# Optimization experiments

Hardware: AMD Instinct MI355X
Metric: run time of the kernel (lower is better)

## Reference

```python
import jax, jax.numpy as jnp
from jax import lax
import numpy as np

B, D, L = 32, 64, 4096
E = 8          # num_experts
K = 2          # top-k
OC = 32        # out_channels


def setup_inputs() -> dict:
    key = jax.random.key(0)
    ks = jax.random.split(key, 6)
    x = jax.random.normal(ks[0], (B, D, L), dtype=jnp.float32)
    # gating weight [D*5, E] (torch init is zeros; use small random for a meaningful reference)
    w_gate = jax.random.normal(ks[1], (D * 5, E), dtype=jnp.float32) * 0.02
    # Conv1d(D -> OC, kernel 3)
    conv1_w = jax.random.normal(ks[2], (OC, D, 3), dtype=jnp.float32) * (1.0 / np.sqrt(D * 3))
    conv1_b = jax.random.normal(ks[3], (OC,), dtype=jnp.float32) * 0.01
    # Conv1d(OC -> OC*E, kernel 1)
    conv2_w = jax.random.normal(ks[4], (OC * E, OC, 1), dtype=jnp.float32) * (1.0 / np.sqrt(OC))
    conv2_b = jax.random.normal(ks[5], (OC * E,), dtype=jnp.float32) * 0.01
    return {"x": x, "w_gate": w_gate, "conv1_w": conv1_w, "conv1_b": conv1_b,
            "conv2_w": conv2_w, "conv2_b": conv2_b}


def _gates(g_in, w_gate):
    # eval-mode noisy_top_k_gating: no noise, softmax -> top-(k+1) -> renormalize top-k -> scatter
    logits = jax.nn.softmax(g_in @ w_gate, axis=1)            # [B, E]
    top_v, top_i = lax.top_k(logits, min(K + 1, E))           # sorted descending
    vk = top_v[:, :K]
    ik = top_i[:, :K]
    gk = vk / (jnp.sum(vk, axis=1, keepdims=True) + 1e-6)
    gates = jnp.zeros_like(logits).at[jnp.arange(logits.shape[0])[:, None], ik].set(gk)
    return gates


def reference(x, w_gate, conv1_w, conv1_b, conv2_w, conv2_b):
    b, d, l = x.shape
    g_in = x[:, :, -6:-1].reshape(b, d * 5)                   # last-5-timestep gating features
    gates = _gates(g_in, w_gate)                              # [B, E]
    dn = ("NCH", "OIH", "NCH")
    h = lax.conv_general_dilated(x, conv1_w, (1,), "VALID", dimension_numbers=dn)
    h = jnp.tanh(h + conv1_b[None, :, None])                  # [B, OC, L-2]
    out = lax.conv_general_dilated(h, conv2_w, (1,), "VALID", dimension_numbers=dn)
    out = out + conv2_b[None, :, None]                        # [B, OC*E, L']
    lp = out.shape[-1]
    out = out.transpose(0, 2, 1).reshape(b, lp, OC, E)        # [B, L', OC, E]
    moe = jnp.einsum("blde,be->bld", out, gates)              # weighted combine
    return moe.transpose(0, 2, 1)                             # [B, OC, L']
```

## Files before the change

### kernel.cpp

```cpp
#include <hip/hip_runtime.h>
#include <math.h>

#define B_  32
#define D_  64
#define L_  4096
#define E_  8
#define OC_ 32
#define LP_ 4094

typedef __attribute__((ext_vector_type(8)))  short short8;
typedef __attribute__((ext_vector_type(16))) float float16;

static __device__ __forceinline__ unsigned cvtpk(float a, float b) {
    unsigned r;
    asm("v_cvt_pk_bf16_f32 %0, %1, %2" : "=v"(r) : "v"(a), "v"(b));
    return r;
}
static __device__ __forceinline__ float fast_tanh(float x) {
    float e = __expf(2.0f * x);
    return fmaf(-2.0f, __builtin_amdgcn_rcpf(e + 1.0f), 1.0f);
}

static __device__ __forceinline__ void compute_tile(
    const unsigned short* __restrict__ xbuf,
    const short8* a1, const short8* a2,
    const float* __restrict__ c1b,
    const float* __restrict__ c2b,
    int i0, int i1, float g0, float g1,
    float* __restrict__ outb,
    int l0, int wv, int cl, int hi)
{
    const int cb = wv * 32;
    float16 acc = (float16)0.0f;
    #pragma unroll
    for (int t = 0; t < 3; ++t) {
        int row = cb + cl + t;
        int rb  = row * 128;
        int swz = (row & 7) << 4;
        #pragma unroll
        for (int q = 0; q < 4; ++q) {
            int off = (rb + q * 32 + hi * 16) ^ swz;
            short8 bf = *(const short8*)((const char*)xbuf + off);
            acc = __builtin_amdgcn_mfma_f32_32x32x16_bf16(a1[t * 4 + q], bf, acc, 0, 0, 0);
        }
    }

    float th[16];
    #pragma unroll
    for (int r = 0; r < 16; ++r) {
        int row = (r & 3) + 8 * (r >> 2) + 4 * hi;
        th[r] = fast_tanh(acc[r] + c1b[row]);
    }

    unsigned x0a = hi ? cvtpk(th[0],  th[1])  : cvtpk(th[4],  th[5]);
    unsigned x0b = hi ? cvtpk(th[2],  th[3])  : cvtpk(th[6],  th[7]);
    unsigned x1a = hi ? cvtpk(th[8],  th[9])  : cvtpk(th[12], th[13]);
    unsigned x1b = hi ? cvtpk(th[10], th[11]) : cvtpk(th[14], th[15]);
    unsigned r0a = (unsigned)__shfl_xor((int)x0a, 32, 64);
    unsigned r0b = (unsigned)__shfl_xor((int)x0b, 32, 64);
    unsigned r1a = (unsigned)__shfl_xor((int)x1a, 32, 64);
    unsigned r1b = (unsigned)__shfl_xor((int)x1b, 32, 64);

    union U { short8 s8; unsigned u[4]; };
    U b0, b1;
    b0.u[0] = hi ? r0a : cvtpk(th[0], th[1]);
    b0.u[1] = hi ? r0b : cvtpk(th[2], th[3]);
    b0.u[2] = hi ? cvtpk(th[4], th[5]) : r0a;
    b0.u[3] = hi ? cvtpk(th[6], th[7]) : r0b;
    b1.u[0] = hi ? r1a : cvtpk(th[8], th[9]);
    b1.u[1] = hi ? r1b : cvtpk(th[10], th[11]);
    b1.u[2] = hi ? cvtpk(th[12], th[13]) : r1a;
    b1.u[3] = hi ? cvtpk(th[14], th[15]) : r1b;

    float16 acc2 = (float16)0.0f;
    acc2 = __builtin_amdgcn_mfma_f32_32x32x16_bf16(a2[0], b0.s8, acc2, 0, 0, 0);
    acc2 = __builtin_amdgcn_mfma_f32_32x32x16_bf16(a2[1], b1.s8, acc2, 0, 0, 0);

    int l = l0 + cb + cl;
    if (l < LP_) {
        float* ob = outb + l;
        #pragma unroll
        for (int r = 0; r < 16; ++r) {
            int row = (r & 3) + 8 * (r >> 2) + 4 * hi;
            float bb = fmaf(g0, c2b[row * E_ + i0], g1 * c2b[row * E_ + i1]);
            ob[(size_t)row * LP_] = acc2[r] + bb;
        }
    }
}

__global__ __launch_bounds__(512, 1)
void fused_all(const float* __restrict__ x,
               const float* __restrict__ w_gate,
               const float* __restrict__ c1w,
               const float* __restrict__ c1b,
               const float* __restrict__ c2w,
               const float* __restrict__ c2b,
               float* __restrict__ out)
{
    __shared__ __align__(16) unsigned short xT0[260 * 64];
    __shared__ __align__(16) unsigned short xT1[260 * 64];
    __shared__ __align__(16) unsigned short aFl[12 * 64 * 8];
    __shared__ __align__(16) unsigned short a2L[2 * 64 * 8];
    __shared__ float gF[2];
    __shared__ int   gI[2];

    const int tid  = threadIdx.x;
    const int lane = tid & 63;
    const int wv   = tid >> 6;
    const int b    = blockIdx.x >> 3;
    const int S    = (blockIdx.x & 7) << 9;
    const float* xb = x + (size_t)b * (D_ * L_);

    const int c2 = tid >> 4;
    const int jb = (tid & 15) << 2;
    const float* p0 = xb + (size_t)(2 * c2) * L_;
    const float* p1 = p0 + L_;
    const int haloc = tid >> 1;
    const int haloj = tid & 1;

    float4 A0[4], A1[4], B0[4], B1[4];
    #pragma unroll
    for (int jq = 0; jq < 4; ++jq) {
        int j = S + jq * 64 + jb;
        A0[jq] = *(const float4*)(p0 + j);
        A1[jq] = *(const float4*)(p1 + j);
        B0[jq] = *(const float4*)(p0 + 256 + j);
        B1[jq] = *(const float4*)(p1 + 256 + j);
    }
    float hA0 = 0.f, hA1 = 0.f, hB0 = 0.f, hB1 = 0.f;
    if (tid < 64) {
        int lgA = S + 256 + haloj;
        hA0 = xb[(size_t)(2 * haloc) * L_ + lgA];
        hA1 = xb[(size_t)(2 * haloc + 1) * L_ + lgA];
        int lgB = S + 512 + haloj;
        if (lgB > L_ - 1) lgB = L_ - 1;
        hB0 = xb[(size_t)(2 * haloc) * L_ + lgB];
        hB1 = xb[(size_t)(2 * haloc + 1) * L_ + lgB];
    }

    const int tid2 = tid - 256;
    const int w_oc = tid2 >> 3;
    const int w_c0 = (tid2 & 7) << 3;
    float wv24[24];
    if (tid >= 256) {
        const float* wp = c1w + w_oc * 192 + w_c0 * 3;
        #pragma unroll
        for (int q = 0; q < 6; ++q)
            *(float4*)(wv24 + 4 * q) = *(const float4*)(wp + 4 * q);
    }

    if (wv == 0) {
        const int d = lane;
        float part[E_];
        #pragma unroll
        for (int e = 0; e < E_; ++e) part[e] = 0.f;
        #pragma unroll
        for (int t = 0; t < 5; ++t) {
            float xvt = xb[(size_t)d * L_ + (L_ - 6) + t];
            const float* wgp = w_gate + (d * 5 + t) * E_;
            float4 wa = *(const float4*)wgp;
            float4 wb = *(const float4*)(wgp + 4);
            part[0] = fmaf(xvt, wa.x, part[0]);
            part[1] = fmaf(xvt, wa.y, part[1]);
            part[2] = fmaf(xvt, wa.z, part[2]);
            part[3] = fmaf(xvt, wa.w, part[3]);
            part[4] = fmaf(xvt, wb.x, part[4]);
            part[5] = fmaf(xvt, wb.y, part[5]);
            part[6] = fmaf(xvt, wb.z, part[6]);
            part[7] = fmaf(xvt, wb.w, part[7]);
        }
        #pragma unroll
        for (int off = 1; off < 64; off <<= 1) {
            #pragma unroll
            for (int e = 0; e < E_; ++e)
                part[e] += __shfl_xor(part[e], off, 64);
        }
        float m = part[0];
        #pragma unroll
        for (int e = 1; e < E_; ++e) m = fmaxf(m, part[e]);
        float p[E_], s = 0.f;
        #pragma unroll
        for (int e = 0; e < E_; ++e) { p[e] = expf(part[e] - m); s += p[e]; }
        float inv = 1.f / s;
        #pragma unroll
        for (int e = 0; e < E_; ++e) p[e] *= inv;

        int i0 = 0;
        #pragma unroll
        for (int e = 1; e < E_; ++e) if (p[e] > p[i0]) i0 = e;
        int i1 = (i0 == 0) ? 1 : 0;
        #pragma unroll
        for (int e = 0; e < E_; ++e) {
            if (e == i0) continue;
            if (p[e] > p[i1]) i1 = e;
        }
        const float v0 = p[i0], v1 = p[i1];
        const float den = v0 + v1 + 1e-6f;
        const float g0 = v0 / den, g1 = v1 / den;

        const int cl0 = lane & 31;
        const int hi0 = lane >> 5;
        #pragma unroll
        for (int ks = 0; ks < 2; ++ks) {
            const float* q0 = c2w + (cl0 * E_ + i0) * OC_ + ks * 16 + hi0 * 8;
            const float* q1 = c2w + (cl0 * E_ + i1) * OC_ + ks * 16 + hi0 * 8;
            float4 u0a = *(const float4*)q0, u0b = *(const float4*)(q0 + 4);
            float4 u1a = *(const float4*)q1, u1b = *(const float4*)(q1 + 4);
            union { short8 s8; unsigned u[4]; } f;
            f.u[0] = cvtpk(fmaf(g0, u0a.x, g1 * u1a.x), fmaf(g0, u0a.y, g1 * u1a.y));
            f.u[1] = cvtpk(fmaf(g0, u0a.z, g1 * u1a.z), fmaf(g0, u0a.w, g1 * u1a.w));
            f.u[2] = cvtpk(fmaf(g0, u0b.x, g1 * u1b.x), fmaf(g0, u0b.y, g1 * u1b.y));
            f.u[3] = cvtpk(fmaf(g0, u0b.z, g1 * u1b.z), fmaf(g0, u0b.w, g1 * u1b.w));
            *(short8*)(a2L + (ks * 64 + lane) * 8) = f.s8;
        }
        if (lane == 0) {
            gF[0] = g0; gF[1] = g1;
            gI[0] = i0; gI[1] = i1;
        }
    }

    if (tid >= 256) {
        const int ksoff = w_c0 >> 4;
        const int half  = (w_c0 >> 3) & 1;
        #pragma unroll
        for (int t = 0; t < 3; ++t) {
            union { short8 s8; unsigned u[4]; } w8;
            #pragma unroll
            for (int jj = 0; jj < 4; ++jj)
                w8.u[jj] = cvtpk(wv24[(2 * jj) * 3 + t], wv24[(2 * jj + 1) * 3 + t]);
            int base = ((t * 4 + ksoff) * 64 + half * 32 + w_oc) * 8;
            *(short8*)(aFl + base) = w8.s8;
        }
    }

    #pragma unroll
    for (int jq = 0; jq < 4; ++jq) {
        float e0[4] = {A0[jq].x, A0[jq].y, A0[jq].z, A0[jq].w};
        float e1[4] = {A1[jq].x, A1[jq].y, A1[jq].z, A1[jq].w};
        float f0[4] = {B0[jq].x, B0[jq].y, B0[jq].z, B0[jq].w};
        float f1[4] = {B1[jq].x, B1[jq].y, B1[jq].z, B1[jq].w};
        #pragma unroll
        for (int r = 0; r < 4; ++r) {
            int row = jq * 64 + jb + r;
            int off = (row * 128 + c2 * 4) ^ ((row & 7) << 4);
            *(unsigned*)((char*)xT0 + off) = cvtpk(e0[r], e1[r]);
            *(unsigned*)((char*)xT1 + off) = cvtpk(f0[r], f1[r]);
        }
    }
    if (tid < 64) {
        int row = 256 + haloj;
        int off = (row * 128 + haloc * 4) ^ ((row & 7) << 4);
        *(unsigned*)((char*)xT0 + off) = cvtpk(hA0, hA1);
        *(unsigned*)((char*)xT1 + off) = cvtpk(hB0, hB1);
    }

    __syncthreads();

    const int cl = lane & 31;
    const int hi = lane >> 5;
    short8 a1[12];
    #pragma unroll
    for (int ks = 0; ks < 12; ++ks)
        a1[ks] = *(const short8*)(aFl + (ks * 64 + lane) * 8);
    short8 a2[2];
    a2[0] = *(const short8*)(a2L + (0 * 64 + lane) * 8);
    a2[1] = *(const short8*)(a2L + (1 * 64 + lane) * 8);
    const float g0 = gF[0], g1 = gF[1];
    const int   i0 = gI[0], i1 = gI[1];

    float* outb = out + (size_t)b * (OC_ * (size_t)LP_);

    compute_tile(xT0, a1, a2, c1b, c2b, i0, i1, g0, g1, outb, S,       wv, cl, hi);
    compute_tile(xT1, a1, a2, c1b, c2b, i0, i1, g0, g1, outb, S + 256, wv, cl, hi);
}

extern "C" void kernel_launch(void* const* d_in, const int* in_sizes, int n_in,
                              void* d_out, int out_size, void* d_ws, size_t ws_size,
                              hipStream_t stream)
{
    const float* x      = (const float*)d_in[0];
    const float* w_gate = (const float*)d_in[1];
    const float* c1w    = (const float*)d_in[2];
    const float* c1b    = (const float*)d_in[3];
    const float* c2w    = (const float*)d_in[4];
    const float* c2b    = (const float*)d_in[5];
    float* out = (float*)d_out;

    fused_all<<<B_ * 8, 512, 0, stream>>>(x, w_gate, c1w, c1b, c2w, c2b, out);
}
```

Before: 19.46 us.

## Stage second x tile during first compute and move gating wave off staging

Only the first 256-column tile is loaded and converted before the barrier. The second tile's global loads are issued early, but their conversion into LDS is deferred until after the first compute_tile and guarded by an extra barrier, so that load latency overlaps compute. Staging work moves to waves 1-7, leaving wave 0 to do only the gating, and conv1 weight prep shifts to threads 64-319. The cost is an extra __syncthreads, registers held live across the first compute, and an uneven load split across threads.

```diff
diff --git a/kernel.cpp b/kernel.cpp
--- a/kernel.cpp
+++ b/kernel.cpp
@@ -111,38 +111,37 @@
     const int S    = (blockIdx.x & 7) << 9;
     const float* xb = x + (size_t)b * (D_ * L_);
 
-    const int c2 = tid >> 4;
-    const int jb = (tid & 15) << 2;
-    const float* p0 = xb + (size_t)(2 * c2) * L_;
-    const float* p1 = p0 + L_;
-    const int haloc = tid >> 1;
-    const int haloj = tid & 1;
-
-    float4 A0[4], A1[4], B0[4], B1[4];
-    #pragma unroll
-    for (int jq = 0; jq < 4; ++jq) {
-        int j = S + jq * 64 + jb;
-        A0[jq] = *(const float4*)(p0 + j);
-        A1[jq] = *(const float4*)(p1 + j);
-        B0[jq] = *(const float4*)(p0 + 256 + j);
-        B1[jq] = *(const float4*)(p1 + 256 + j);
-    }
-    float hA0 = 0.f, hA1 = 0.f, hB0 = 0.f, hB1 = 0.f;
-    if (tid < 64) {
-        int lgA = S + 256 + haloj;
-        hA0 = xb[(size_t)(2 * haloc) * L_ + lgA];
-        hA1 = xb[(size_t)(2 * haloc + 1) * L_ + lgA];
-        int lgB = S + 512 + haloj;
-        if (lgB > L_ - 1) lgB = L_ - 1;
-        hB0 = xb[(size_t)(2 * haloc) * L_ + lgB];
-        hB1 = xb[(size_t)(2 * haloc + 1) * L_ + lgB];
-    }
-
-    const int tid2 = tid - 256;
-    const int w_oc = tid2 >> 3;
-    const int w_c0 = (tid2 & 7) << 3;
+    const bool stager = (tid >= 64);
+    const int  t1 = tid - 64;
+    const int  nit = stager ? (4 + (t1 < 256 ? 1 : 0)) : 0;
+    int ic2[5], ijc[5];
+    float4 A0[5], A1[5], B0[5], B1[5];
+
+    #pragma unroll
+    for (int k = 0; k < 5; ++k) {
+        if (k < nit) {
+            int i = t1 + k * 448;
+            ic2[k] = i >> 6;
+            ijc[k] = (i & 63) << 2;
+            const float* p0 = xb + (size_t)(2 * ic2[k]) * L_ + S + ijc[k];
+            A0[k] = *(const float4*)p0;
+            A1[k] = *(const float4*)(p0 + L_);
+        }
+    }
+    float hA0 = 0.f, hA1 = 0.f;
+    const int t7 = tid - 448;
+    if (t7 >= 0) {
+        int haloc = t7 >> 1, haloj = t7 & 1;
+        int lg = S + 256 + haloj;
+        hA0 = xb[(size_t)(2 * haloc) * L_ + lg];
+        hA1 = xb[(size_t)(2 * haloc + 1) * L_ + lg];
+    }
+
+    const int t2 = tid - 64;
+    const int w_oc = t2 >> 3;
+    const int w_c0 = (t2 & 7) << 3;
     float wv24[24];
-    if (tid >= 256) {
+    if (tid >= 64 && tid < 320) {
         const float* wp = c1w + w_oc * 192 + w_c0 * 3;
         #pragma unroll
         for (int q = 0; q < 6; ++q)
@@ -219,7 +218,44 @@
         }
     }
 
-    if (tid >= 256) {
+    #pragma unroll
+    for (int k = 0; k < 5; ++k) {
+        if (k < nit) {
+            float e0[4] = {A0[k].x, A0[k].y, A0[k].z, A0[k].w};
+            float e1[4] = {A1[k].x, A1[k].y, A1[k].z, A1[k].w};
+            #pragma unroll
+            for (int r = 0; r < 4; ++r) {
+                int row = ijc[k] + r;
+                int off = (row * 128 + ic2[k] * 4) ^ ((row & 7) << 4);
+                *(unsigned*)((char*)xT0 + off) = cvtpk(e0[r], e1[r]);
+            }
+        }
+    }
+    if (t7 >= 0) {
+        int haloc = t7 >> 1, haloj = t7 & 1;
+        int row = 256 + haloj;
+        int off = (row * 128 + haloc * 4) ^ ((row & 7) << 4);
+        *(unsigned*)((char*)xT0 + off) = cvtpk(hA0, hA1);
+    }
+
+    #pragma unroll
+    for (int k = 0; k < 5; ++k) {
+        if (k < nit) {
+            const float* p0 = xb + (size_t)(2 * ic2[k]) * L_ + S + 256 + ijc[k];
+            B0[k] = *(const float4*)p0;
+            B1[k] = *(const float4*)(p0 + L_);
+        }
+    }
+    float hB0 = 0.f, hB1 = 0.f;
+    if (t7 >= 0) {
+        int haloc = t7 >> 1, haloj = t7 & 1;
+        int lg = S + 512 + haloj;
+        if (lg > L_ - 1) lg = L_ - 1;
+        hB0 = xb[(size_t)(2 * haloc) * L_ + lg];
+        hB1 = xb[(size_t)(2 * haloc + 1) * L_ + lg];
+    }
+
+    if (tid >= 64 && tid < 320) {
         const int ksoff = w_c0 >> 4;
         const int half  = (w_c0 >> 3) & 1;
         #pragma unroll
@@ -233,27 +269,6 @@
         }
     }
 
-    #pragma unroll
-    for (int jq = 0; jq < 4; ++jq) {
-        float e0[4] = {A0[jq].x, A0[jq].y, A0[jq].z, A0[jq].w};
-        float e1[4] = {A1[jq].x, A1[jq].y, A1[jq].z, A1[jq].w};
-        float f0[4] = {B0[jq].x, B0[jq].y, B0[jq].z, B0[jq].w};
-        float f1[4] = {B1[jq].x, B1[jq].y, B1[jq].z, B1[jq].w};
-        #pragma unroll
-        for (int r = 0; r < 4; ++r) {
-            int row = jq * 64 + jb + r;
-            int off = (row * 128 + c2 * 4) ^ ((row & 7) << 4);
-            *(unsigned*)((char*)xT0 + off) = cvtpk(e0[r], e1[r]);
-            *(unsigned*)((char*)xT1 + off) = cvtpk(f0[r], f1[r]);
-        }
-    }
-    if (tid < 64) {
-        int row = 256 + haloj;
-        int off = (row * 128 + haloc * 4) ^ ((row & 7) << 4);
-        *(unsigned*)((char*)xT0 + off) = cvtpk(hA0, hA1);
-        *(unsigned*)((char*)xT1 + off) = cvtpk(hB0, hB1);
-    }
-
     __syncthreads();
 
     const int cl = lane & 31;
@@ -270,7 +285,30 @@
 
     float* outb = out + (size_t)b * (OC_ * (size_t)LP_);
 
-    compute_tile(xT0, a1, a2, c1b, c2b, i0, i1, g0, g1, outb, S,       wv, cl, hi);
+    compute_tile(xT0, a1, a2, c1b, c2b, i0, i1, g0, g1, outb, S, wv, cl, hi);
+
+    #pragma unroll
+    for (int k = 0; k < 5; ++k) {
+        if (k < nit) {
+            float f0[4] = {B0[k].x, B0[k].y, B0[k].z, B0[k].w};
+            float f1[4] = {B1[k].x, B1[k].y, B1[k].z, B1[k].w};
+            #pragma unroll
+            for (int r = 0; r < 4; ++r) {
+                int row = ijc[k] + r;
+                int off = (row * 128 + ic2[k] * 4) ^ ((row & 7) << 4);
+                *(unsigned*)((char*)xT1 + off) = cvtpk(f0[r], f1[r]);
+            }
+        }
+    }
+    if (t7 >= 0) {
+        int haloc = t7 >> 1, haloj = t7 & 1;
+        int row = 256 + haloj;
+        int off = (row * 128 + haloc * 4) ^ ((row & 7) << 4);
+        *(unsigned*)((char*)xT1 + off) = cvtpk(hB0, hB1);
+    }
+
+    __syncthreads();
+
     compute_tile(xT1, a1, a2, c1b, c2b, i0, i1, g0, g1, outb, S + 256, wv, cl, hi);
 }
 
```

Result: slower. 21.45 us (+10.2%).
